# Kernel tuning notes

Hardware: AMD Instinct MI355X
Metric: run time of the kernel (lower is better)

The kernel has to match this reference:

```python
import jax, jax.numpy as jnp
import numpy as np
from jax import lax

T, B, D_IN, H, D_OUT = 512, 64, 256, 512, 256


def _lstm_scan(xs, h0, c0, Wih, Whh, b):
    """Standard LSTM over time. xs: [T,B,Din]; returns (hs [T,B,H], hT, cT).
    Gate order i,f,g,o (PyTorch convention)."""
    def step(carry, x_t):
        h, c = carry
        gates = x_t @ Wih.T + h @ Whh.T + b            # [B, 4H]
        i, f, g, o = jnp.split(gates, 4, axis=-1)
        i = jax.nn.sigmoid(i)
        f = jax.nn.sigmoid(f)
        g = jnp.tanh(g)
        o = jax.nn.sigmoid(o)
        c = f * c + i * g
        h = o * jnp.tanh(c)
        return (h, c), h
    (hT, cT), hs = lax.scan(step, (h0, c0), xs)
    return hs, hT, cT


def setup_inputs() -> dict:
    key = jax.random.key(0)
    ks = jax.random.split(key, 10)
    s = 0.05
    return {
        "x": jax.random.normal(ks[0], (T, B, D_IN), jnp.float32),
        "target": jax.random.uniform(ks[1], (T, B, D_OUT), jnp.float32),
        "hidden_state": jnp.zeros((1, B, H), jnp.float32),
        "cell_state": jnp.zeros((1, B, H), jnp.float32),
        "enc_Wih": jax.random.normal(ks[2], (4 * H, D_IN), jnp.float32) * s,
        "enc_Whh": jax.random.normal(ks[3], (4 * H, H), jnp.float32) * s,
        "enc_b": jax.random.normal(ks[4], (4 * H,), jnp.float32) * s,
        "dec_Wih": jax.random.normal(ks[5], (4 * H, D_OUT), jnp.float32) * s,
        "dec_Whh": jax.random.normal(ks[6], (4 * H, H), jnp.float32) * s,
        "dec_b": jax.random.normal(ks[7], (4 * H,), jnp.float32) * s,
        "fc_W": jax.random.normal(ks[8], (D_OUT, H), jnp.float32) * s,
        "fc_b": jax.random.normal(ks[9], (D_OUT,), jnp.float32) * s,
    }


def reference(x, target, hidden_state, cell_state,
              enc_Wih, enc_Whh, enc_b, dec_Wih, dec_Whh, dec_b, fc_W, fc_b):
    # Encoder: consume x, keep final (h, c).
    _, h, c = _lstm_scan(x, hidden_state[0], cell_state[0], enc_Wih, enc_Whh, enc_b)
    # Decoder with teacher_forcing = 1.0: input at step t is target[t-1],
    # step 0 input is zeros (matches torch code's initial x = zeros).
    dec_in = jnp.concatenate([jnp.zeros((1,) + target.shape[1:], target.dtype),
                              target[:-1]], axis=0)          # [T, B, D_OUT]
    hs, _, _ = _lstm_scan(dec_in, h, c, dec_Wih, dec_Whh, dec_b)  # [T, B, H]
    logits = hs @ fc_W.T + fc_b                                   # [T, B, D_OUT]
    return jax.nn.softmax(logits, axis=-1)
```

## Files before the change

kernel.cpp:

```cpp
#include <hip/hip_runtime.h>
#include <math.h>

#define TT 512
#define BB 64
#define DIN 256
#define HH 512
#define DOUT 256

#define RSU 388
#define RSH 776

#define A_HI_OFF 0
#define A_LO_OFF 6208
#define P_OFF    12416
#define B_OFF    13696
#define C_OFF    13728
#define HST_HI   13856
#define HST_LO   13920
#define SMEM_U32 13984
#define SMEM_BYTES (SMEM_U32*4)

#define FCS 516

typedef _Float16 f16x8 __attribute__((ext_vector_type(8)));
typedef float    f32x4 __attribute__((ext_vector_type(4)));
typedef unsigned u32x4 __attribute__((ext_vector_type(4)));

union H16 { _Float16 f; unsigned short u; };
__device__ __forceinline__ unsigned short f16bits(_Float16 h) { H16 t; t.f = h; return t.u; }

__device__ __forceinline__ void pack2(float x, float y, unsigned& hi, unsigned& lo) {
    _Float16 hx = (_Float16)x, hy = (_Float16)y;
    _Float16 lx = (_Float16)((x - (float)hx) * 2048.0f);
    _Float16 ly = (_Float16)((y - (float)hy) * 2048.0f);
    hi = (unsigned)f16bits(hx) | ((unsigned)f16bits(hy) << 16);
    lo = (unsigned)f16bits(lx) | ((unsigned)f16bits(ly) << 16);
}

__device__ __forceinline__ u32x4 ld16_cohere(const void* p) {
    u32x4 v;
    asm volatile("global_load_dwordx4 %0, %1, off sc0 sc1"
                 : "=&v"(v) : "v"(p) : "memory");
    return v;
}
__device__ __forceinline__ void st16_cohere(void* p, u32x4 v) {
    asm volatile("global_store_dwordx4 %0, %1, off sc0 sc1"
                 :: "v"(p), "v"(v) : "memory");
}

__device__ __forceinline__ bool tag_ok(u32x4 v, unsigned par) {
    unsigned a = v[0] & v[1] & v[2] & v[3];
    unsigned o = v[0] | v[1] | v[2] | v[3];
    unsigned x = par ? ~a : o;
    return (x & 0x00010001u) == 0u;
}

__device__ __forceinline__ void load_w_regs(const float* __restrict__ Whh,
                                            const float* __restrict__ Wih,
                                            int u0, int ct, int kh, int m, int q,
                                            f16x8* __restrict__ wh, f16x8* __restrict__ wl) {
    const int r = ct*16 + m;
    const int C = (r >> 3)*HH + u0 + (r & 7);
    const float* rowH = Whh + (size_t)C*HH;
    const float* rowI = Wih + (size_t)C*DIN;
    #pragma unroll
    for (int j = 0; j < 12; ++j) {
        const int k0 = (kh*12 + j)*32 + q*8;
        const float* src = (k0 < 512) ? (rowH + k0) : (rowI + (k0 - 512));
        float4 a = ((const float4*)src)[0];
        float4 b = ((const float4*)src)[1];
        f16x8 h8, l8;
        _Float16 t;
        t = (_Float16)a.x; h8[0]=t; l8[0]=(_Float16)((a.x-(float)t)*2048.0f);
        t = (_Float16)a.y; h8[1]=t; l8[1]=(_Float16)((a.y-(float)t)*2048.0f);
        t = (_Float16)a.z; h8[2]=t; l8[2]=(_Float16)((a.z-(float)t)*2048.0f);
        t = (_Float16)a.w; h8[3]=t; l8[3]=(_Float16)((a.w-(float)t)*2048.0f);
        t = (_Float16)b.x; h8[4]=t; l8[4]=(_Float16)((b.x-(float)t)*2048.0f);
        t = (_Float16)b.y; h8[5]=t; l8[5]=(_Float16)((b.y-(float)t)*2048.0f);
        t = (_Float16)b.z; h8[6]=t; l8[6]=(_Float16)((b.z-(float)t)*2048.0f);
        t = (_Float16)b.w; h8[7]=t; l8[7]=(_Float16)((b.w-(float)t)*2048.0f);
        wh[j] = h8; wl[j] = l8;
    }
}

__device__ __forceinline__ void stage_x_f16(unsigned* __restrict__ sm32,
                                            const float* __restrict__ src, int tid) {
    for (int r = 0; r < 4; ++r) {
        int idx4 = tid + 256*r;
        int b = idx4 >> 6, j4 = idx4 & 63;
        float4 v = ((const float4*)(src + (size_t)b*DIN))[j4];
        unsigned h0, l0, h1, l1;
        pack2(v.x, v.y, h0, l0);
        pack2(v.z, v.w, h1, l1);
        int o = b*RSU + 256 + 2*j4;
        sm32[A_HI_OFF + o]     = h0;
        sm32[A_HI_OFF + o + 1] = h1;
        sm32[A_LO_OFF + o]     = l0;
        sm32[A_LO_OFF + o + 1] = l1;
    }
}

__device__ __forceinline__ void stage_x_zero_f16(unsigned* __restrict__ sm32, int tid) {
    for (int r = 0; r < 4; ++r) {
        int idx4 = tid + 256*r;
        int b = idx4 >> 6, j4 = idx4 & 63;
        int o = b*RSU + 256 + 2*j4;
        sm32[A_HI_OFF + o]     = 0u;
        sm32[A_HI_OFF + o + 1] = 0u;
        sm32[A_LO_OFF + o]     = 0u;
        sm32[A_LO_OFF + o + 1] = 0u;
    }
}

__global__ __launch_bounds__(256, 1)
void lstm_persist(const float* __restrict__ x, const float* __restrict__ target,
                  const float* __restrict__ h0, const float* __restrict__ c0,
                  const float* __restrict__ eWih, const float* __restrict__ eWhh,
                  const float* __restrict__ eb,
                  const float* __restrict__ dWih, const float* __restrict__ dWhh,
                  const float* __restrict__ db,
                  float* __restrict__ hs,
                  unsigned short* __restrict__ hbh,
                  unsigned short* __restrict__ hbl)
{
    extern __shared__ unsigned sm32[];
    float* p_l = (float*)(sm32 + P_OFF);
    float* b_l = (float*)(sm32 + B_OFF);
    float* c_l = (float*)(sm32 + C_OFF);
    unsigned* hst_hi = sm32 + HST_HI;
    unsigned* hst_lo = sm32 + HST_LO;

    const int tid = (int)threadIdx.x;
    const int xcd = (int)(blockIdx.x & 7);
    const int ib  = xcd >> 1;
    const int sub = xcd & 1;
    const int ij  = (int)(blockIdx.x >> 3) | (sub << 5);
    const int b0  = ib * 16;
    const int u0  = ij * 8;

    if (tid < 128) {
        int b = tid >> 3, u = tid & 7;
        c_l[tid] = c0[(size_t)(b0 + b)*HH + u0 + u];
    }
    if (tid < 32) b_l[tid] = eb[(tid >> 3)*HH + u0 + (tid & 7)];
    stage_x_f16(sm32, x + (size_t)b0*DIN, tid);
    for (int r = 0; r < 8; ++r) {
        int idx4 = tid + 256*r;
        int b = idx4 >> 7, j4 = idx4 & 127;
        float4 v = ((const float4*)(h0 + (size_t)(b0 + b)*HH))[j4];
        unsigned h0p, l0p, h1p, l1p;
        pack2(v.x, v.y, h0p, l0p);
        pack2(v.z, v.w, h1p, l1p);
        int o = b*RSU + 2*j4;
        sm32[A_HI_OFF + o]     = h0p;
        sm32[A_HI_OFF + o + 1] = h1p;
        sm32[A_LO_OFF + o]     = l0p;
        sm32[A_LO_OFF + o + 1] = l1p;
    }
    __syncthreads();

    const int lane = tid & 63;
    const int wid  = tid >> 6;
    const int m    = lane & 15;
    const int q    = lane >> 4;
    const int ct   = wid & 1;
    const int kh   = wid >> 1;

    const _Float16* aH = (const _Float16*)(sm32 + A_HI_OFF);
    const _Float16* aL = (const _Float16*)(sm32 + A_LO_OFF);
    const int aoff = m*RSH + q*8;

    f16x8 w_hi[12], w_lo[12];
    load_w_regs(eWhh, eWih, u0, ct, kh, m, q, w_hi, w_lo);

    for (int s = 0; s < 1024; ++s) {
        f32x4 Chh = {0.f, 0.f, 0.f, 0.f};
        f32x4 Chl = {0.f, 0.f, 0.f, 0.f};
        f32x4 Clh = {0.f, 0.f, 0.f, 0.f};
        {
            const int ks0 = kh * 12;
            #pragma unroll
            for (int j = 0; j < 12; ++j) {
                const int o = (ks0 + j) * 32;
                f16x8 ah = *(const f16x8*)(aH + aoff + o);
                f16x8 al = *(const f16x8*)(aL + aoff + o);
                Chh = __builtin_amdgcn_mfma_f32_16x16x32_f16(ah, w_hi[j], Chh, 0, 0, 0);
                Chl = __builtin_amdgcn_mfma_f32_16x16x32_f16(ah, w_lo[j], Chl, 0, 0, 0);
                Clh = __builtin_amdgcn_mfma_f32_16x16x32_f16(al, w_hi[j], Clh, 0, 0, 0);
            }
        }
        {
            float4 C;
            const float sc = 1.0f / 2048.0f;
            C.x = Chh[0] + (Chl[0] + Clh[0]) * sc;
            C.y = Chh[1] + (Chl[1] + Clh[1]) * sc;
            C.z = Chh[2] + (Chl[2] + Clh[2]) * sc;
            C.w = Chh[3] + (Chl[3] + Clh[3]) * sc;
            *(float4*)(p_l + (ct*2 + kh)*320 + m*20 + q*4) = C;
        }
        __syncthreads();

        const unsigned par = (unsigned)(((s + 1) >> 1) & 1);

        float hval = 0.f;
        if (tid < 128) {
            int b = tid >> 3, u = tid & 7;
            float gi = p_l[      u*20 + b] + p_l[320 +      u*20 + b] + b_l[u];
            float gf = p_l[(8+u)*20 + b] + p_l[320 + (8+u)*20 + b] + b_l[8 + u];
            float gg = p_l[640 +   u*20 + b] + p_l[960 +      u*20 + b] + b_l[16 + u];
            float go = p_l[640 + (8+u)*20 + b] + p_l[960 + (8+u)*20 + b] + b_l[24 + u];
            float ii = 1.f / (1.f + expf(-gi));
            float ff = 1.f / (1.f + expf(-gf));
            float g2 = tanhf(gg);
            float oo = 1.f / (1.f + expf(-go));
            float c  = ff * c_l[tid] + ii * g2;
            c_l[tid] = c;
            hval = oo * tanhf(c);
            _Float16 hh = (_Float16)hval;
            unsigned uh = ((unsigned)f16bits(hh) & 0xFFFEu) | par;
            H16 th; th.u = (unsigned short)uh;
            _Float16 hl = (_Float16)((hval - (float)th.f) * 2048.0f);
            unsigned ul = ((unsigned)f16bits(hl) & 0xFFFEu) | par;
            ((unsigned short*)hst_hi)[tid] = (unsigned short)uh;
            ((unsigned short*)hst_lo)[tid] = (unsigned short)ul;
        }
        __syncthreads();

        if (tid < 32) {
            asm volatile("s_waitcnt vmcnt(0)" ::: "memory");
            int b    = tid & 15;
            int isLo = tid >> 4;
            u32x4 v = *(const u32x4*)((isLo ? hst_lo : hst_hi) + b*4);
            unsigned short* base = isLo ? hbl : hbh;
            st16_cohere(base + ((size_t)(((s & 1) ^ 1))*BB + b0 + b)*HH + u0, v);
        }

        if (s >= 512 && tid < 128) {
            int b = tid >> 3, u = tid & 7;
            hs[((size_t)(s - 512)*BB + (b0 + b))*HH + (u0 + u)] = hval;
        }
        if (s == 511) {
            load_w_regs(dWhh, dWih, u0, ct, kh, m, q, w_hi, w_lo);
            if (tid < 32) b_l[tid] = db[(tid >> 3)*HH + u0 + (tid & 7)];
        }
        {
            int ns = s + 1;
            if (ns < 1024) {
                if (ns == 512)       stage_x_zero_f16(sm32, tid);
                else if (ns < 512)   stage_x_f16(sm32, x + ((size_t)ns*BB + b0)*DIN, tid);
                else                 stage_x_f16(sm32, target + ((size_t)(ns - 513)*BB + b0)*DOUT, tid);
            }
        }

        if (s < 1023) {
            const unsigned short* srcH = hbh + (size_t)((s + 1) & 1)*BB*HH + (size_t)b0*HH;
            const unsigned short* srcL = hbl + (size_t)((s + 1) & 1)*BB*HH + (size_t)b0*HH;
            u32x4 h0v = {0,0,0,0}, h1v = {0,0,0,0}, h2v = {0,0,0,0}, h3v = {0,0,0,0};
            u32x4 l0v = {0,0,0,0}, l1v = {0,0,0,0}, l2v = {0,0,0,0}, l3v = {0,0,0,0};
            unsigned pend = 0xFFu;
            do {
                if (pend & 0x01u) h0v = ld16_cohere((const u32x4*)srcH + tid);
                if (pend & 0x02u) h1v = ld16_cohere((const u32x4*)srcH + tid + 256);
                if (pend & 0x04u) h2v = ld16_cohere((const u32x4*)srcH + tid + 512);
                if (pend & 0x08u) h3v = ld16_cohere((const u32x4*)srcH + tid + 768);
                if (pend & 0x10u) l0v = ld16_cohere((const u32x4*)srcL + tid);
                if (pend & 0x20u) l1v = ld16_cohere((const u32x4*)srcL + tid + 256);
                if (pend & 0x40u) l2v = ld16_cohere((const u32x4*)srcL + tid + 512);
                if (pend & 0x80u) l3v = ld16_cohere((const u32x4*)srcL + tid + 768);
                asm volatile("s_waitcnt vmcnt(0)"
                             : "+v"(h0v), "+v"(h1v), "+v"(h2v), "+v"(h3v),
                               "+v"(l0v), "+v"(l1v), "+v"(l2v), "+v"(l3v) :: "memory");
                if (tag_ok(h0v, par)) pend &= ~0x01u;
                if (tag_ok(h1v, par)) pend &= ~0x02u;
                if (tag_ok(h2v, par)) pend &= ~0x04u;
                if (tag_ok(h3v, par)) pend &= ~0x08u;
                if (tag_ok(l0v, par)) pend &= ~0x10u;
                if (tag_ok(l1v, par)) pend &= ~0x20u;
                if (tag_ok(l2v, par)) pend &= ~0x40u;
                if (tag_ok(l3v, par)) pend &= ~0x80u;
            } while (pend);
            {
                int idx, b, j0;
                idx = tid;       b = idx >> 6; j0 = (idx & 63)*4;
                *(u32x4*)(sm32 + A_HI_OFF + b*RSU + j0) = h0v;
                *(u32x4*)(sm32 + A_LO_OFF + b*RSU + j0) = l0v;
                idx = tid + 256; b = idx >> 6; j0 = (idx & 63)*4;
                *(u32x4*)(sm32 + A_HI_OFF + b*RSU + j0) = h1v;
                *(u32x4*)(sm32 + A_LO_OFF + b*RSU + j0) = l1v;
                idx = tid + 512; b = idx >> 6; j0 = (idx & 63)*4;
                *(u32x4*)(sm32 + A_HI_OFF + b*RSU + j0) = h2v;
                *(u32x4*)(sm32 + A_LO_OFF + b*RSU + j0) = l2v;
                idx = tid + 768; b = idx >> 6; j0 = (idx & 63)*4;
                *(u32x4*)(sm32 + A_HI_OFF + b*RSU + j0) = h3v;
                *(u32x4*)(sm32 + A_LO_OFF + b*RSU + j0) = l3v;
            }
        }
        __syncthreads();
    }
}

__global__ __launch_bounds__(256, 1)
void fc_kernel(const float* __restrict__ hs, const float* __restrict__ W,
               const float* __restrict__ bias, float* __restrict__ out)
{
    extern __shared__ float sm[];
    float* hs_l = sm;
    float* w_l  = sm + 16*FCS;

    const int tid = (int)threadIdx.x;
    const int rb = (int)(blockIdx.x >> 3);
    const int cb = (int)(blockIdx.x & 7);

    for (int r = 0; r < 8; ++r) {
        int id = tid + 256*r;
        int b = id >> 7, j = id & 127;
        float4 v = ((const float4*)(hs + (size_t)(rb*16 + b)*HH))[j];
        *(float4*)(hs_l + b*FCS + 4*j) = v;
    }
    for (int r = 0; r < 16; ++r) {
        int id = tid + 256*r;
        int c = id >> 7, j = id & 127;
        float4 v = ((const float4*)(W + (size_t)(cb*32 + c)*HH))[j];
        *(float4*)(w_l + c*FCS + 4*j) = v;
    }
    __syncthreads();

    const int kc = tid & 7, bt = (tid >> 3) & 3, ct = tid >> 5;
    float acc[4][4] = {};
    const float* ap = hs_l + (bt*4)*FCS + 4*kc;
    const float* wp = w_l  + (ct*4)*FCS + 4*kc;
    #pragma unroll 4
    for (int i = 0; i < 16; ++i) {
        float4 av[4], wv[4];
        #pragma unroll
        for (int q = 0; q < 4; ++q) av[q] = *(const float4*)(ap + q*FCS + 32*i);
        #pragma unroll
        for (int q = 0; q < 4; ++q) wv[q] = *(const float4*)(wp + q*FCS + 32*i);
        #pragma unroll
        for (int b2 = 0; b2 < 4; ++b2)
            #pragma unroll
            for (int c2 = 0; c2 < 4; ++c2)
                acc[b2][c2] += av[b2].x*wv[c2].x + av[b2].y*wv[c2].y
                             + av[b2].z*wv[c2].z + av[b2].w*wv[c2].w;
    }
    #pragma unroll
    for (int b2 = 0; b2 < 4; ++b2)
        #pragma unroll
        for (int c2 = 0; c2 < 4; ++c2) {
            float v = acc[b2][c2];
            v += __shfl_xor(v, 1, 64);
            v += __shfl_xor(v, 2, 64);
            v += __shfl_xor(v, 4, 64);
            acc[b2][c2] = v;
        }
    if (kc == 0) {
        #pragma unroll
        for (int b2 = 0; b2 < 4; ++b2)
            #pragma unroll
            for (int c2 = 0; c2 < 4; ++c2) {
                int row = rb*16 + bt*4 + b2;
                int col = cb*32 + ct*4 + c2;
                out[(size_t)row*DOUT + col] = acc[b2][c2] + bias[col];
            }
    }
}

__global__ __launch_bounds__(256, 1)
void softmax_kernel(float* __restrict__ out)
{
    int row  = (int)blockIdx.x * 4 + ((int)threadIdx.x >> 6);
    int lane = (int)threadIdx.x & 63;
    float4 v = ((const float4*)(out + (size_t)row*DOUT))[lane];
    float m = fmaxf(fmaxf(v.x, v.y), fmaxf(v.z, v.w));
    #pragma unroll
    for (int d = 1; d < 64; d <<= 1) m = fmaxf(m, __shfl_xor(m, d, 64));
    float ex = expf(v.x - m), ey = expf(v.y - m), ez = expf(v.z - m), ew = expf(v.w - m);
    float ssum = ex + ey + ez + ew;
    #pragma unroll
    for (int d = 1; d < 64; d <<= 1) ssum += __shfl_xor(ssum, d, 64);
    float inv = 1.f / ssum;
    float4 o = make_float4(ex*inv, ey*inv, ez*inv, ew*inv);
    ((float4*)(out + (size_t)row*DOUT))[lane] = o;
}

__global__ void init_kernel(unsigned* __restrict__ hbh32, unsigned* __restrict__ hbl32)
{
    int i = (int)blockIdx.x * 256 + (int)threadIdx.x;
    unsigned* base = (i < 8192) ? hbh32 : hbl32;
    int j = (i & 8191) * 4;
    unsigned val = (j < 16384) ? 0u : 0x00010001u;
    u32x4 v = {val, val, val, val};
    *(u32x4*)(base + j) = v;
}

extern "C" void kernel_launch(void* const* d_in, const int* in_sizes, int n_in,
                              void* d_out, int out_size, void* d_ws, size_t ws_size,
                              hipStream_t stream) {
    (void)in_sizes; (void)n_in; (void)out_size; (void)ws_size;
    const float* x      = (const float*)d_in[0];
    const float* target = (const float*)d_in[1];
    const float* h0     = (const float*)d_in[2];
    const float* c0     = (const float*)d_in[3];
    const float* eWih   = (const float*)d_in[4];
    const float* eWhh   = (const float*)d_in[5];
    const float* eb     = (const float*)d_in[6];
    const float* dWih   = (const float*)d_in[7];
    const float* dWhh   = (const float*)d_in[8];
    const float* db     = (const float*)d_in[9];
    const float* fcW    = (const float*)d_in[10];
    const float* fcb    = (const float*)d_in[11];
    float* out = (float*)d_out;

    float* hs = (float*)d_ws + 1024;
    unsigned short* hbh = (unsigned short*)(hs + (size_t)TT*BB*HH);
    unsigned short* hbl = hbh + (size_t)2*BB*HH;

    init_kernel<<<dim3(64), dim3(256), 0, stream>>>((unsigned*)hbh, (unsigned*)hbl);

    lstm_persist<<<dim3(256), dim3(256), SMEM_BYTES, stream>>>(
        x, target, h0, c0, eWih, eWhh, eb, dWih, dWhh, db, hs, hbh, hbl);

    size_t lds_fc = (size_t)(48*FCS) * sizeof(float);
    fc_kernel<<<dim3(16384), dim3(256), lds_fc, stream>>>(hs, fcW, fcb, out);

    softmax_kernel<<<dim3(8192), dim3(256), 0, stream>>>(out);
}
```

Before: 4.308 ms.

## Repartition persistent LSTM blocks to 8 batch rows by 16 hidden units

```diff
diff --git a/kernel.cpp b/kernel.cpp
--- a/kernel.cpp
+++ b/kernel.cpp
@@ -9,15 +9,16 @@
 
 #define RSU 388
 #define RSH 776
+#define PST 68
 
 #define A_HI_OFF 0
 #define A_LO_OFF 6208
 #define P_OFF    12416
-#define B_OFF    13696
-#define C_OFF    13728
-#define HST_HI   13856
-#define HST_LO   13920
-#define SMEM_U32 13984
+#define B_OFF    13504
+#define C_OFF    13568
+#define HST_HI   13696
+#define HST_LO   13760
+#define SMEM_U32 13824
 #define SMEM_BYTES (SMEM_U32*4)
 
 #define FCS 516
@@ -58,34 +59,37 @@
 __device__ __forceinline__ void load_w_regs(const float* __restrict__ Whh,
                                             const float* __restrict__ Wih,
                                             int u0, int ct, int kh, int m, int q,
-                                            f16x8* __restrict__ wh, f16x8* __restrict__ wl) {
-    const int r = ct*16 + m;
-    const int C = (r >> 3)*HH + u0 + (r & 7);
-    const float* rowH = Whh + (size_t)C*HH;
-    const float* rowI = Wih + (size_t)C*DIN;
+                                            f16x8 (&whi)[2][12], f16x8 (&wlo)[2][12]) {
     #pragma unroll
-    for (int j = 0; j < 12; ++j) {
-        const int k0 = (kh*12 + j)*32 + q*8;
-        const float* src = (k0 < 512) ? (rowH + k0) : (rowI + (k0 - 512));
-        float4 a = ((const float4*)src)[0];
-        float4 b = ((const float4*)src)[1];
-        f16x8 h8, l8;
-        _Float16 t;
-        t = (_Float16)a.x; h8[0]=t; l8[0]=(_Float16)((a.x-(float)t)*2048.0f);
-        t = (_Float16)a.y; h8[1]=t; l8[1]=(_Float16)((a.y-(float)t)*2048.0f);
-        t = (_Float16)a.z; h8[2]=t; l8[2]=(_Float16)((a.z-(float)t)*2048.0f);
-        t = (_Float16)a.w; h8[3]=t; l8[3]=(_Float16)((a.w-(float)t)*2048.0f);
-        t = (_Float16)b.x; h8[4]=t; l8[4]=(_Float16)((b.x-(float)t)*2048.0f);
-        t = (_Float16)b.y; h8[5]=t; l8[5]=(_Float16)((b.y-(float)t)*2048.0f);
-        t = (_Float16)b.z; h8[6]=t; l8[6]=(_Float16)((b.z-(float)t)*2048.0f);
-        t = (_Float16)b.w; h8[7]=t; l8[7]=(_Float16)((b.w-(float)t)*2048.0f);
-        wh[j] = h8; wl[j] = l8;
+    for (int t = 0; t < 2; ++t) {
+        const int col = ct*32 + t*16 + m;
+        const int C   = (col >> 4)*HH + u0 + (col & 15);
+        const float* rowH = Whh + (size_t)C*HH;
+        const float* rowI = Wih + (size_t)C*DIN;
+        #pragma unroll
+        for (int j = 0; j < 12; ++j) {
+            const int ks = kh*12 + j;
+            const float* src = (ks < 16) ? (rowH + ks*32 + q*8)
+                                         : (rowI + (ks - 16)*32 + q*8);
+            float4 a = ((const float4*)src)[0];
+            float4 b = ((const float4*)src)[1];
+            f16x8 h8, l8; _Float16 t16;
+            t16=(_Float16)a.x; h8[0]=t16; l8[0]=(_Float16)((a.x-(float)t16)*2048.0f);
+            t16=(_Float16)a.y; h8[1]=t16; l8[1]=(_Float16)((a.y-(float)t16)*2048.0f);
+            t16=(_Float16)a.z; h8[2]=t16; l8[2]=(_Float16)((a.z-(float)t16)*2048.0f);
+            t16=(_Float16)a.w; h8[3]=t16; l8[3]=(_Float16)((a.w-(float)t16)*2048.0f);
+            t16=(_Float16)b.x; h8[4]=t16; l8[4]=(_Float16)((b.x-(float)t16)*2048.0f);
+            t16=(_Float16)b.y; h8[5]=t16; l8[5]=(_Float16)((b.y-(float)t16)*2048.0f);
+            t16=(_Float16)b.z; h8[6]=t16; l8[6]=(_Float16)((b.z-(float)t16)*2048.0f);
+            t16=(_Float16)b.w; h8[7]=t16; l8[7]=(_Float16)((b.w-(float)t16)*2048.0f);
+            whi[t][j] = h8; wlo[t][j] = l8;
+        }
     }
 }
 
 __device__ __forceinline__ void stage_x_f16(unsigned* __restrict__ sm32,
                                             const float* __restrict__ src, int tid) {
-    for (int r = 0; r < 4; ++r) {
+    for (int r = 0; r < 2; ++r) {
         int idx4 = tid + 256*r;
         int b = idx4 >> 6, j4 = idx4 & 63;
         float4 v = ((const float4*)(src + (size_t)b*DIN))[j4];
@@ -101,10 +105,10 @@
 }
 
 __device__ __forceinline__ void stage_x_zero_f16(unsigned* __restrict__ sm32, int tid) {
-    for (int r = 0; r < 4; ++r) {
-        int idx4 = tid + 256*r;
-        int b = idx4 >> 6, j4 = idx4 & 63;
-        int o = b*RSU + 256 + 2*j4;
+    for (int r = 0; r < 2; ++r) {
+        int idx = tid + 256*r;
+        int row = idx >> 6, j = idx & 63;
+        int o = row*RSU + 256 + 2*j;
         sm32[A_HI_OFF + o]     = 0u;
         sm32[A_HI_OFF + o + 1] = 0u;
         sm32[A_LO_OFF + o]     = 0u;
@@ -131,20 +135,22 @@
     unsigned* hst_lo = sm32 + HST_LO;
 
     const int tid = (int)threadIdx.x;
-    const int xcd = (int)(blockIdx.x & 7);
-    const int ib  = xcd >> 1;
-    const int sub = xcd & 1;
-    const int ij  = (int)(blockIdx.x >> 3) | (sub << 5);
-    const int b0  = ib * 16;
-    const int u0  = ij * 8;
+    const int g   = (int)(blockIdx.x & 7);
+    const int ij  = (int)(blockIdx.x >> 3);
+    const int b0  = g * 8;
+    const int u0  = ij * 16;
 
     if (tid < 128) {
-        int b = tid >> 3, u = tid & 7;
+        int b = tid >> 4, u = tid & 15;
         c_l[tid] = c0[(size_t)(b0 + b)*HH + u0 + u];
     }
-    if (tid < 32) b_l[tid] = eb[(tid >> 3)*HH + u0 + (tid & 7)];
+    if (tid < 64) b_l[tid] = eb[(tid >> 4)*HH + u0 + (tid & 15)];
+    for (int i = tid; i < 8*RSU; i += 256) {
+        sm32[A_HI_OFF + 8*RSU + i] = 0u;
+        sm32[A_LO_OFF + 8*RSU + i] = 0u;
+    }
     stage_x_f16(sm32, x + (size_t)b0*DIN, tid);
-    for (int r = 0; r < 8; ++r) {
+    for (int r = 0; r < 4; ++r) {
         int idx4 = tid + 256*r;
         int b = idx4 >> 7, j4 = idx4 & 127;
         float4 v = ((const float4*)(h0 + (size_t)(b0 + b)*HH))[j4];
@@ -168,35 +174,33 @@
 
     const _Float16* aH = (const _Float16*)(sm32 + A_HI_OFF);
     const _Float16* aL = (const _Float16*)(sm32 + A_LO_OFF);
-    const int aoff = m*RSH + q*8;
-
-    f16x8 w_hi[12], w_lo[12];
-    load_w_regs(eWhh, eWih, u0, ct, kh, m, q, w_hi, w_lo);
+    const int abase = m*RSH + q*8 + (kh*12)*32;
+
+    f16x8 whi[2][12], wlo[2][12];
+    load_w_regs(eWhh, eWih, u0, ct, kh, m, q, whi, wlo);
 
     for (int s = 0; s < 1024; ++s) {
-        f32x4 Chh = {0.f, 0.f, 0.f, 0.f};
-        f32x4 Chl = {0.f, 0.f, 0.f, 0.f};
-        f32x4 Clh = {0.f, 0.f, 0.f, 0.f};
-        {
-            const int ks0 = kh * 12;
+        f32x4 hh0 = {0.f,0.f,0.f,0.f}, hl0 = {0.f,0.f,0.f,0.f}, lh0 = {0.f,0.f,0.f,0.f};
+        f32x4 hh1 = {0.f,0.f,0.f,0.f}, hl1 = {0.f,0.f,0.f,0.f}, lh1 = {0.f,0.f,0.f,0.f};
+        #pragma unroll
+        for (int j = 0; j < 12; ++j) {
+            f16x8 ah = *(const f16x8*)(aH + abase + j*32);
+            f16x8 al = *(const f16x8*)(aL + abase + j*32);
+            hh0 = __builtin_amdgcn_mfma_f32_16x16x32_f16(ah, whi[0][j], hh0, 0, 0, 0);
+            hl0 = __builtin_amdgcn_mfma_f32_16x16x32_f16(ah, wlo[0][j], hl0, 0, 0, 0);
+            lh0 = __builtin_amdgcn_mfma_f32_16x16x32_f16(al, whi[0][j], lh0, 0, 0, 0);
+            hh1 = __builtin_amdgcn_mfma_f32_16x16x32_f16(ah, whi[1][j], hh1, 0, 0, 0);
+            hl1 = __builtin_amdgcn_mfma_f32_16x16x32_f16(ah, wlo[1][j], hl1, 0, 0, 0);
+            lh1 = __builtin_amdgcn_mfma_f32_16x16x32_f16(al, whi[1][j], lh1, 0, 0, 0);
+        }
+        if (q < 2) {
+            const float sc = 1.0f/2048.0f;
+            float* pb = p_l + (kh*8 + q*4)*PST + ct*32 + m;
             #pragma unroll
-            for (int j = 0; j < 12; ++j) {
-                const int o = (ks0 + j) * 32;
-                f16x8 ah = *(const f16x8*)(aH + aoff + o);
-                f16x8 al = *(const f16x8*)(aL + aoff + o);
-                Chh = __builtin_amdgcn_mfma_f32_16x16x32_f16(ah, w_hi[j], Chh, 0, 0, 0);
-                Chl = __builtin_amdgcn_mfma_f32_16x16x32_f16(ah, w_lo[j], Chl, 0, 0, 0);
-                Clh = __builtin_amdgcn_mfma_f32_16x16x32_f16(al, w_hi[j], Clh, 0, 0, 0);
+            for (int i = 0; i < 4; ++i) {
+                pb[i*PST]      = hh0[i] + (hl0[i] + lh0[i])*sc;
+                pb[i*PST + 16] = hh1[i] + (hl1[i] + lh1[i])*sc;
             }
-        }
-        {
-            float4 C;
-            const float sc = 1.0f / 2048.0f;
-            C.x = Chh[0] + (Chl[0] + Clh[0]) * sc;
-            C.y = Chh[1] + (Chl[1] + Clh[1]) * sc;
-            C.z = Chh[2] + (Chl[2] + Clh[2]) * sc;
-            C.w = Chh[3] + (Chl[3] + Clh[3]) * sc;
-            *(float4*)(p_l + (ct*2 + kh)*320 + m*20 + q*4) = C;
         }
         __syncthreads();
 
@@ -204,22 +208,24 @@
 
         float hval = 0.f;
         if (tid < 128) {
-            int b = tid >> 3, u = tid & 7;
-            float gi = p_l[      u*20 + b] + p_l[320 +      u*20 + b] + b_l[u];
-            float gf = p_l[(8+u)*20 + b] + p_l[320 + (8+u)*20 + b] + b_l[8 + u];
-            float gg = p_l[640 +   u*20 + b] + p_l[960 +      u*20 + b] + b_l[16 + u];
-            float go = p_l[640 + (8+u)*20 + b] + p_l[960 + (8+u)*20 + b] + b_l[24 + u];
-            float ii = 1.f / (1.f + expf(-gi));
-            float ff = 1.f / (1.f + expf(-gf));
+            const int b = tid >> 4, u = tid & 15;
+            float gi = b_l[u], gf = b_l[16+u], gg = b_l[32+u], go = b_l[48+u];
+            #pragma unroll
+            for (int ps = 0; ps < 2; ++ps) {
+                const float* pp = p_l + (ps*8 + b)*PST;
+                gi += pp[u]; gf += pp[16+u]; gg += pp[32+u]; go += pp[48+u];
+            }
+            float ii = 1.f/(1.f + expf(-gi));
+            float ff = 1.f/(1.f + expf(-gf));
             float g2 = tanhf(gg);
-            float oo = 1.f / (1.f + expf(-go));
-            float c  = ff * c_l[tid] + ii * g2;
+            float oo = 1.f/(1.f + expf(-go));
+            float c  = ff*c_l[tid] + ii*g2;
             c_l[tid] = c;
-            hval = oo * tanhf(c);
+            hval = oo*tanhf(c);
             _Float16 hh = (_Float16)hval;
             unsigned uh = ((unsigned)f16bits(hh) & 0xFFFEu) | par;
-            H16 th; th.u = (unsigned short)uh;
-            _Float16 hl = (_Float16)((hval - (float)th.f) * 2048.0f);
+            H16 t16; t16.u = (unsigned short)uh;
+            _Float16 hl = (_Float16)((hval - (float)t16.f) * 2048.0f);
             unsigned ul = ((unsigned)f16bits(hl) & 0xFFFEu) | par;
             ((unsigned short*)hst_hi)[tid] = (unsigned short)uh;
             ((unsigned short*)hst_lo)[tid] = (unsigned short)ul;
@@ -228,20 +234,21 @@
 
         if (tid < 32) {
             asm volatile("s_waitcnt vmcnt(0)" ::: "memory");
-            int b    = tid & 15;
-            int isLo = tid >> 4;
-            u32x4 v = *(const u32x4*)((isLo ? hst_lo : hst_hi) + b*4);
-            unsigned short* base = isLo ? hbl : hbh;
-            st16_cohere(base + ((size_t)(((s & 1) ^ 1))*BB + b0 + b)*HH + u0, v);
+            const int idx = tid & 15, isLo = tid >> 4;
+            const int b = idx >> 1, h16 = idx & 1;
+            u32x4 v = *(const u32x4*)((isLo ? hst_lo : hst_hi) + b*8 + h16*4);
+            unsigned short* base = (isLo ? hbl : hbh)
+                + ((size_t)((s & 1) ^ 1)*BB + b0 + b)*HH + u0 + h16*8;
+            st16_cohere(base, v);
         }
 
         if (s >= 512 && tid < 128) {
-            int b = tid >> 3, u = tid & 7;
+            int b = tid >> 4, u = tid & 15;
             hs[((size_t)(s - 512)*BB + (b0 + b))*HH + (u0 + u)] = hval;
         }
         if (s == 511) {
-            load_w_regs(dWhh, dWih, u0, ct, kh, m, q, w_hi, w_lo);
-            if (tid < 32) b_l[tid] = db[(tid >> 3)*HH + u0 + (tid & 7)];
+            load_w_regs(dWhh, dWih, u0, ct, kh, m, q, whi, wlo);
+            if (tid < 64) b_l[tid] = db[(tid >> 4)*HH + u0 + (tid & 15)];
         }
         {
             int ns = s + 1;
@@ -253,47 +260,30 @@
         }
 
         if (s < 1023) {
-            const unsigned short* srcH = hbh + (size_t)((s + 1) & 1)*BB*HH + (size_t)b0*HH;
-            const unsigned short* srcL = hbl + (size_t)((s + 1) & 1)*BB*HH + (size_t)b0*HH;
-            u32x4 h0v = {0,0,0,0}, h1v = {0,0,0,0}, h2v = {0,0,0,0}, h3v = {0,0,0,0};
-            u32x4 l0v = {0,0,0,0}, l1v = {0,0,0,0}, l2v = {0,0,0,0}, l3v = {0,0,0,0};
-            unsigned pend = 0xFFu;
+            const int slot = (s + 1) & 1;
+            const u32x4* SH = (const u32x4*)(hbh + (size_t)slot*BB*HH + (size_t)b0*HH);
+            const u32x4* SL = (const u32x4*)(hbl + (size_t)slot*BB*HH + (size_t)b0*HH);
+            u32x4 v0 = {0,0,0,0}, v1 = {0,0,0,0}, v2 = {0,0,0,0}, v3 = {0,0,0,0};
+            unsigned pend = 0xFu; int tries = 0;
             do {
-                if (pend & 0x01u) h0v = ld16_cohere((const u32x4*)srcH + tid);
-                if (pend & 0x02u) h1v = ld16_cohere((const u32x4*)srcH + tid + 256);
-                if (pend & 0x04u) h2v = ld16_cohere((const u32x4*)srcH + tid + 512);
-                if (pend & 0x08u) h3v = ld16_cohere((const u32x4*)srcH + tid + 768);
-                if (pend & 0x10u) l0v = ld16_cohere((const u32x4*)srcL + tid);
-                if (pend & 0x20u) l1v = ld16_cohere((const u32x4*)srcL + tid + 256);
-                if (pend & 0x40u) l2v = ld16_cohere((const u32x4*)srcL + tid + 512);
-                if (pend & 0x80u) l3v = ld16_cohere((const u32x4*)srcL + tid + 768);
+                if (pend & 1u) v0 = ld16_cohere(SH + tid);
+                if (pend & 2u) v1 = ld16_cohere(SH + tid + 256);
+                if (pend & 4u) v2 = ld16_cohere(SL + tid);
+                if (pend & 8u) v3 = ld16_cohere(SL + tid + 256);
                 asm volatile("s_waitcnt vmcnt(0)"
-                             : "+v"(h0v), "+v"(h1v), "+v"(h2v), "+v"(h3v),
-                               "+v"(l0v), "+v"(l1v), "+v"(l2v), "+v"(l3v) :: "memory");
-                if (tag_ok(h0v, par)) pend &= ~0x01u;
-                if (tag_ok(h1v, par)) pend &= ~0x02u;
-                if (tag_ok(h2v, par)) pend &= ~0x04u;
-                if (tag_ok(h3v, par)) pend &= ~0x08u;
-                if (tag_ok(l0v, par)) pend &= ~0x10u;
-                if (tag_ok(l1v, par)) pend &= ~0x20u;
-                if (tag_ok(l2v, par)) pend &= ~0x40u;
-                if (tag_ok(l3v, par)) pend &= ~0x80u;
+                             : "+v"(v0), "+v"(v1), "+v"(v2), "+v"(v3) :: "memory");
+                if (tag_ok(v0, par)) pend &= ~1u;
+                if (tag_ok(v1, par)) pend &= ~2u;
+                if (tag_ok(v2, par)) pend &= ~4u;
+                if (tag_ok(v3, par)) pend &= ~8u;
+                ++tries;
+                if (pend && tries > 4) __builtin_amdgcn_s_sleep(1);
             } while (pend);
-            {
-                int idx, b, j0;
-                idx = tid;       b = idx >> 6; j0 = (idx & 63)*4;
-                *(u32x4*)(sm32 + A_HI_OFF + b*RSU + j0) = h0v;
-                *(u32x4*)(sm32 + A_LO_OFF + b*RSU + j0) = l0v;
-                idx = tid + 256; b = idx >> 6; j0 = (idx & 63)*4;
-                *(u32x4*)(sm32 + A_HI_OFF + b*RSU + j0) = h1v;
-                *(u32x4*)(sm32 + A_LO_OFF + b*RSU + j0) = l1v;
-                idx = tid + 512; b = idx >> 6; j0 = (idx & 63)*4;
-                *(u32x4*)(sm32 + A_HI_OFF + b*RSU + j0) = h2v;
-                *(u32x4*)(sm32 + A_LO_OFF + b*RSU + j0) = l2v;
-                idx = tid + 768; b = idx >> 6; j0 = (idx & 63)*4;
-                *(u32x4*)(sm32 + A_HI_OFF + b*RSU + j0) = h3v;
-                *(u32x4*)(sm32 + A_LO_OFF + b*RSU + j0) = l3v;
-            }
+            const int j = tid & 63, r0 = tid >> 6;
+            *(u32x4*)(sm32 + A_HI_OFF + (r0    )*RSU + j*4) = v0;
+            *(u32x4*)(sm32 + A_HI_OFF + (r0 + 4)*RSU + j*4) = v1;
+            *(u32x4*)(sm32 + A_LO_OFF + (r0    )*RSU + j*4) = v2;
+            *(u32x4*)(sm32 + A_LO_OFF + (r0 + 4)*RSU + j*4) = v3;
         }
         __syncthreads();
     }
@@ -390,7 +380,7 @@
     int j = (i & 8191) * 4;
     unsigned val = (j < 16384) ? 0u : 0x00010001u;
     u32x4 v = {val, val, val, val};
-    *(u32x4*)(base + j) = v;
+    st16_cohere(base + j, v);
 }
 
 extern "C" void kernel_launch(void* const* d_in, const int* in_sizes, int n_in,
```

After: 5.501 ms. 27.7% more time.
